# Optimization experiments

Measured on AMD Instinct MI355X. Metric: run time of the kernel, lower is better.

Reference implementation:

```python
import jax, jax.numpy as jnp
import numpy as np

B, S, H, HKV, D = 2, 1024, 32, 8, 128


def _rope_tables(seq_len, head_dim, base=10000.0):
    inv_freq = 1.0 / (base ** (np.arange(0, head_dim, 2, dtype=np.float32) / head_dim))
    freqs = np.arange(seq_len, dtype=np.float32)[:, None] * inv_freq[None, :]  # [S, D/2]
    emb = np.concatenate([freqs, freqs], axis=-1)  # [S, D] (Llama layout)
    return jnp.asarray(np.cos(emb)), jnp.asarray(np.sin(emb))


def setup_inputs() -> dict:
    key = jax.random.key(0)
    kq, kk, kv = jax.random.split(key, 3)
    q = jax.random.normal(kq, (B, S, H, D), dtype=jnp.float32)
    k = jax.random.normal(kk, (B, S, HKV, D), dtype=jnp.float32)
    v = jax.random.normal(kv, (B, S, HKV, D), dtype=jnp.float32)
    cos, sin = _rope_tables(S, D)
    # additive causal mask [B, 1, S, S]: 0 where allowed, large negative where masked
    causal = jnp.tril(jnp.ones((S, S), dtype=bool))
    mask = jnp.where(causal, 0.0, -1e9).astype(jnp.float32)
    attention_mask = jnp.broadcast_to(mask[None, None], (B, 1, S, S))
    softmax_scale = 1.0 / float(np.sqrt(D))
    return {
        "query_states": q, "key_states": k, "value_states": v,
        "cos": cos, "sin": sin, "attention_mask": attention_mask,
        "softmax_scale": softmax_scale,
    }


def _apply_rope(x, cos, sin):
    # x: [B, S, h, D]; cos/sin: [S, D]
    d2 = x.shape[-1] // 2
    rot = jnp.concatenate([-x[..., d2:], x[..., :d2]], axis=-1)  # rotate_half
    return x * cos[None, :, None, :] + rot * sin[None, :, None, :]


def reference(query_states, key_states, value_states, cos, sin, attention_mask, softmax_scale):
    b, s, h, d = query_states.shape
    hkv = key_states.shape[2]
    g = h // hkv  # GQA group size
    q = _apply_rope(query_states, cos, sin)
    k = _apply_rope(key_states, cos, sin)
    qg = q.reshape(b, s, hkv, g, d)
    # scores: [B, Hkv, G, Q, K]
    scores = jnp.einsum('bqhgd,bkhd->bhgqk', qg, k) * softmax_scale
    scores = scores + attention_mask[:, :, None]  # [B,1,Q,K] -> broadcast over (Hkv, G)
    p = jax.nn.softmax(scores, axis=-1)
    out = jnp.einsum('bhgqk,bkhd->bqhgd', p, value_states)
    return out.reshape(b, s, h, d)
```

## Files before the change

kernel.cpp:

```cpp
#include <hip/hip_runtime.h>

#define S_LEN 1024
#define D_DIM 128
#define NH    32
#define NKV   8
#define NB    2

typedef __bf16 bf16x8 __attribute__((ext_vector_type(8)));
typedef float  f32x16 __attribute__((ext_vector_type(16)));
typedef unsigned short u16x8 __attribute__((ext_vector_type(8)));
typedef unsigned int   u32x4 __attribute__((ext_vector_type(4)));

__device__ __forceinline__ unsigned short f2bf(float f) {
    unsigned int u = __float_as_uint(f);
    u += 0x7fffu + ((u >> 16) & 1u);
    return (unsigned short)(u >> 16);
}

__device__ __forceinline__ void gld_lds16(const unsigned short* g, unsigned short* l) {
    __builtin_amdgcn_global_load_lds(
        (const __attribute__((address_space(1))) unsigned int*)(g),
        (__attribute__((address_space(3))) unsigned int*)(l), 16, 0, 0);
}

__global__ __launch_bounds__(256) void rope_q_kernel(
    const float* __restrict__ q, const float* __restrict__ cosb,
    const float* __restrict__ sinb, const float* __restrict__ scale_ptr,
    unsigned short* __restrict__ Qr)
{
    const float sc = *scale_ptr * 1.44269504088896f;
    int gid = blockIdx.x * 256 + threadIdx.x;
    int row = gid >> 6;
    int j   = gid & 63;
    int h  = row & (NH - 1);
    int bs = row >> 5;
    int s  = bs & (S_LEN - 1);
    int b  = bs >> 10;
    const float* qp = q + (size_t)row * D_DIM;
    float x0 = qp[j];
    float x1 = qp[j + 64];
    float c  = cosb[s * D_DIM + j];
    float sn = sinb[s * D_DIM + j];
    size_t orow = ((size_t)(b * NH + h) * S_LEN + s) * D_DIM;
    Qr[orow + j]      = f2bf((x0 * c - x1 * sn) * sc);
    Qr[orow + j + 64] = f2bf((x1 * c + x0 * sn) * sc);
}

__global__ __launch_bounds__(256) void rope_k_kernel(
    const float* __restrict__ k, const float* __restrict__ cosb,
    const float* __restrict__ sinb, unsigned short* __restrict__ Kr)
{
    int gid = blockIdx.x * 256 + threadIdx.x;
    int row = gid >> 6;
    int j   = gid & 63;
    int hk = row & (NKV - 1);
    int bs = row >> 3;
    int s  = bs & (S_LEN - 1);
    int b  = bs >> 10;
    const float* kp = k + (size_t)row * D_DIM;
    float x0 = kp[j];
    float x1 = kp[j + 64];
    float c  = cosb[s * D_DIM + j];
    float sn = sinb[s * D_DIM + j];
    size_t orow = ((size_t)(b * NKV + hk) * S_LEN + s) * D_DIM;
    Kr[orow + j]      = f2bf(x0 * c - x1 * sn);
    Kr[orow + j + 64] = f2bf(x1 * c + x0 * sn);
}

__global__ __launch_bounds__(256) void transpose_v_kernel(
    const float* __restrict__ v, unsigned short* __restrict__ Vt)
{
    int blk   = blockIdx.x;
    int stile = blk & 15;
    int hk    = (blk >> 4) & (NKV - 1);
    int b     = blk >> 7;
    int tid   = threadIdx.x;
    __shared__ __align__(16) unsigned short tile[64][132];
#pragma unroll
    for (int i = 0; i < 8; i++) {
        int e    = i * 256 + tid;
        int srow = e >> 5;
        int dq   = (e & 31) * 4;
        const float* vp = v + (((size_t)(b * S_LEN + stile * 64 + srow) * NKV + hk) * D_DIM + dq);
        float4 val = *(const float4*)vp;
        tile[srow][dq + 0] = f2bf(val.x);
        tile[srow][dq + 1] = f2bf(val.y);
        tile[srow][dq + 2] = f2bf(val.z);
        tile[srow][dq + 3] = f2bf(val.w);
    }
    __syncthreads();
    size_t head = (size_t)(b * NKV + hk) * D_DIM * S_LEN;
#pragma unroll
    for (int i = 0; i < 4; i++) {
        int g  = i * 256 + tid;
        int d  = g >> 3;
        int c8 = g & 7;
        int s0 = c8 * 8;
        u16x8 pk;
#pragma unroll
        for (int jj = 0; jj < 8; jj++) pk[jj] = tile[s0 + jj][d];
        *(u16x8*)(Vt + head + (size_t)d * S_LEN + stile * 64 + s0) = pk;
    }
}

__global__ __launch_bounds__(512, 2) void attn_kernel(
    const unsigned short* __restrict__ Qr,
    const unsigned short* __restrict__ Kr,
    const unsigned short* __restrict__ Vt,
    float* __restrict__ out)
{
    const int bid = blockIdx.x;
    const int swz = (bid & 7) * 32 + (bid >> 3);
    const int t  = swz & 3;
    const int h  = (swz >> 2) & 31;
    const int b  = swz >> 7;
    const int hk = h >> 2;

    const int tid  = threadIdx.x;
    const int w    = tid >> 6;
    const int lane = tid & 63;
    const int ln   = lane & 31;
    const int hi   = lane >> 5;

    __shared__ __align__(16) unsigned short Kt[2][64 * 128];
    __shared__ __align__(16) unsigned short Vs[2][128 * 64];

    const int q0 = t * 256 + w * 32;
    const int qg = q0 + ln;

    const unsigned short* khead = Kr + (size_t)(b * NKV + hk) * S_LEN * D_DIM;
    const unsigned short* vhead = Vt + (size_t)(b * NKV + hk) * D_DIM * S_LEN;

    const int krow = lane >> 4;
    const int kcc  = lane & 15;
    const int vrw  = lane >> 3;
    const int vcc  = lane & 7;

    auto stage = [&](int u, int buf) {
        const unsigned short* kt = khead + (size_t)u * 64 * D_DIM;
#pragma unroll
        for (int n = 0; n < 2; n++) {
            int row = w * 8 + n * 4 + krow;
            int cc  = kcc ^ (row & 7);
            gld_lds16(kt + (size_t)row * D_DIM + cc * 8, &Kt[buf][(w * 8 + n * 4) * 128]);
        }
        const unsigned short* vt = vhead + (size_t)u * 64;
#pragma unroll
        for (int n = 0; n < 2; n++) {
            int d  = w * 16 + n * 8 + vrw;
            int cc = vcc ^ (d & 7);
            gld_lds16(vt + (size_t)d * S_LEN + cc * 8, &Vs[buf][(w * 16 + n * 8) * 64]);
        }
    };

    const unsigned short* qrow =
        Qr + ((size_t)(b * NH + h) * S_LEN + qg) * D_DIM + hi * 8;
    bf16x8 qf[8];
#pragma unroll
    for (int dd = 0; dd < 8; dd++)
        qf[dd] = *(const bf16x8*)(qrow + dd * 16);

    f32x16 o[4];
#pragma unroll
    for (int dt = 0; dt < 4; dt++)
#pragma unroll
        for (int r = 0; r < 16; r++) o[dt][r] = 0.f;
    float m_run = -1e30f, lsum = 0.f;

    const int U = 4 * t + 4;
    stage(0, 0);

#pragma unroll 1
    for (int u = 0; u < U; ++u) {
        const int cur = u & 1;
        __syncthreads();
        if (u + 1 < U) stage(u + 1, cur ^ 1);

        if (64 * u <= q0 + 31) {
            const bool act1 = (64 * u + 32 <= q0 + 31);

            f32x16 st[2];
#pragma unroll
            for (int r = 0; r < 16; r++) { st[0][r] = 0.f; st[1][r] = 0.f; }
            __builtin_amdgcn_s_setprio(1);
#pragma unroll
            for (int s = 0; s < 2; s++) {
                if (s == 0 || act1) {
#pragma unroll
                    for (int dd = 0; dd < 8; dd++) {
                        int row = s * 32 + ln;
                        int c   = (2 * dd + hi) ^ (row & 7);
                        bf16x8 kf = *(const bf16x8*)(&Kt[cur][row * 128 + c * 8]);
                        st[s] = __builtin_amdgcn_mfma_f32_32x32x16_bf16(kf, qf[dd], st[s], 0, 0, 0);
                    }
                }
            }
            __builtin_amdgcn_s_setprio(0);

            if (64 * u + 63 > q0) {
#pragma unroll
                for (int s = 0; s < 2; s++)
#pragma unroll
                    for (int r = 0; r < 16; r++) {
                        int kg = 64 * u + 32 * s + (r & 3) + 8 * (r >> 2) + 4 * hi;
                        if (kg > qg) st[s][r] = -1e30f;
                    }
            }

            float mx = -1e30f;
#pragma unroll
            for (int r = 0; r < 16; r++) mx = fmaxf(mx, st[0][r]);
            if (act1) {
#pragma unroll
                for (int r = 0; r < 16; r++) mx = fmaxf(mx, st[1][r]);
            }
            float pm = fmaxf(mx, __shfl_xor(mx, 32));

            if (__any(pm > m_run + 8.f)) {
                float mnew = fmaxf(m_run, pm);
                float ps   = exp2f(m_run - mnew);
                m_run = mnew;
                lsum *= ps;
#pragma unroll
                for (int r = 0; r < 16; r++) {
                    float psr = __shfl(ps, (r & 3) + 8 * (r >> 2) + 4 * hi);
#pragma unroll
                    for (int dt = 0; dt < 4; dt++) o[dt][r] *= psr;
                }
            }
            float ls = 0.f;
#pragma unroll
            for (int r = 0; r < 16; r++) {
                float p = exp2f(st[0][r] - m_run);
                st[0][r] = p; ls += p;
            }
            if (act1) {
#pragma unroll
                for (int r = 0; r < 16; r++) {
                    float p = exp2f(st[1][r] - m_run);
                    st[1][r] = p; ls += p;
                }
            }
            lsum += ls + __shfl_xor(ls, 32);

            const char* vbase = (const char*)&Vs[cur][0];
            __builtin_amdgcn_s_setprio(1);
#pragma unroll
            for (int ks = 0; ks < 4; ks++) {
                if (ks < 2 || act1) {
                    const f32x16& sv = st[ks >> 1];
                    const int g = (ks & 1) * 8;
                    unsigned int d0 = (unsigned)f2bf(sv[g + 0]) | ((unsigned)f2bf(sv[g + 1]) << 16);
                    unsigned int d1 = (unsigned)f2bf(sv[g + 2]) | ((unsigned)f2bf(sv[g + 3]) << 16);
                    unsigned int d2 = (unsigned)f2bf(sv[g + 4]) | ((unsigned)f2bf(sv[g + 5]) << 16);
                    unsigned int d3 = (unsigned)f2bf(sv[g + 6]) | ((unsigned)f2bf(sv[g + 7]) << 16);
                    u32x4 paw = {d0, d1, d2, d3};
                    bf16x8 pa = __builtin_bit_cast(bf16x8, paw);
#pragma unroll
                    for (int dt = 0; dt < 4; dt++) {
                        int d = dt * 32 + ln;
                        const char* vrow = vbase + d * 128;
                        int x = d & 7;
                        uint2 vlo = *(const uint2*)(vrow + (((2 * ks)     ^ x) * 16) + hi * 8);
                        uint2 vhi = *(const uint2*)(vrow + (((2 * ks + 1) ^ x) * 16) + hi * 8);
                        u32x4 vw = {vlo.x, vlo.y, vhi.x, vhi.y};
                        bf16x8 vf = __builtin_bit_cast(bf16x8, vw);
                        o[dt] = __builtin_amdgcn_mfma_f32_32x32x16_bf16(pa, vf, o[dt], 0, 0, 0);
                    }
                }
            }
            __builtin_amdgcn_s_setprio(0);
        }
    }

    float rcp = 1.0f / lsum;
    float* ob = out + ((size_t)(b * S_LEN + q0) * NH + h) * D_DIM;
#pragma unroll
    for (int r = 0; r < 16; r++) {
        int qo = (r & 3) + 8 * (r >> 2) + 4 * hi;
        float invr = __shfl(rcp, qo);
#pragma unroll
        for (int dt = 0; dt < 4; dt++)
            ob[(size_t)qo * NH * D_DIM + dt * 32 + ln] = o[dt][r] * invr;
    }
}

extern "C" void kernel_launch(void* const* d_in, const int* in_sizes, int n_in,
                              void* d_out, int out_size, void* d_ws, size_t ws_size,
                              hipStream_t stream) {
    const float* q    = (const float*)d_in[0];
    const float* k    = (const float*)d_in[1];
    const float* v    = (const float*)d_in[2];
    const float* cosb = (const float*)d_in[3];
    const float* sinb = (const float*)d_in[4];
    const float* scale = (const float*)d_in[6];
    float* out = (float*)d_out;

    unsigned short* Qr = (unsigned short*)d_ws;
    unsigned short* Kr = Qr + (size_t)NB * NH  * S_LEN * D_DIM;
    unsigned short* Vt = Kr + (size_t)NB * NKV * S_LEN * D_DIM;

    rope_q_kernel<<<NB * S_LEN * NH / 4, 256, 0, stream>>>(q, cosb, sinb, scale, Qr);
    rope_k_kernel<<<NB * S_LEN * NKV / 4, 256, 0, stream>>>(k, cosb, sinb, Kr);
    transpose_v_kernel<<<NB * NKV * (S_LEN / 64), 256, 0, stream>>>(v, Vt);
    attn_kernel<<<NB * NH * (S_LEN / 256), 512, 0, stream>>>(Qr, Kr, Vt, out);
}
```

Before: 77.05 us.

## Fuse Q RoPE into attention, merge K/V prep, triple-buffer with paired causal tiles

Removes the separate Q RoPE kernel: each attention wave now loads fp32 Q, cos and sin directly, applies RoPE and the softmax scale, and converts to bf16 in registers. K RoPE and the V transpose are merged into one launch, so the pipeline drops from four launches to two. The attention kernel switches to 256-thread blocks that each handle two 128-row query tiles (qt = 7-pr and qt = pr) to balance causal work, and uses a three-stage K/V LDS ring with explicit vmcnt waits. Costs are a larger LDS footprint, only 256 blocks in the grid, and Q RoPE inputs read in fp32 inside the main kernel.

```diff
diff --git a/kernel.cpp b/kernel.cpp
--- a/kernel.cpp
+++ b/kernel.cpp
@@ -23,98 +23,76 @@
         (__attribute__((address_space(3))) unsigned int*)(l), 16, 0, 0);
 }
 
-__global__ __launch_bounds__(256) void rope_q_kernel(
-    const float* __restrict__ q, const float* __restrict__ cosb,
-    const float* __restrict__ sinb, const float* __restrict__ scale_ptr,
-    unsigned short* __restrict__ Qr)
+__global__ __launch_bounds__(256) void prep_kv_kernel(
+    const float* __restrict__ k, const float* __restrict__ cosb,
+    const float* __restrict__ sinb, const float* __restrict__ v,
+    unsigned short* __restrict__ Kr, unsigned short* __restrict__ Vt)
 {
-    const float sc = *scale_ptr * 1.44269504088896f;
-    int gid = blockIdx.x * 256 + threadIdx.x;
-    int row = gid >> 6;
-    int j   = gid & 63;
-    int h  = row & (NH - 1);
-    int bs = row >> 5;
-    int s  = bs & (S_LEN - 1);
-    int b  = bs >> 10;
-    const float* qp = q + (size_t)row * D_DIM;
-    float x0 = qp[j];
-    float x1 = qp[j + 64];
-    float c  = cosb[s * D_DIM + j];
-    float sn = sinb[s * D_DIM + j];
-    size_t orow = ((size_t)(b * NH + h) * S_LEN + s) * D_DIM;
-    Qr[orow + j]      = f2bf((x0 * c - x1 * sn) * sc);
-    Qr[orow + j + 64] = f2bf((x1 * c + x0 * sn) * sc);
-}
-
-__global__ __launch_bounds__(256) void rope_k_kernel(
-    const float* __restrict__ k, const float* __restrict__ cosb,
-    const float* __restrict__ sinb, unsigned short* __restrict__ Kr)
-{
-    int gid = blockIdx.x * 256 + threadIdx.x;
-    int row = gid >> 6;
-    int j   = gid & 63;
-    int hk = row & (NKV - 1);
-    int bs = row >> 3;
-    int s  = bs & (S_LEN - 1);
-    int b  = bs >> 10;
-    const float* kp = k + (size_t)row * D_DIM;
-    float x0 = kp[j];
-    float x1 = kp[j + 64];
-    float c  = cosb[s * D_DIM + j];
-    float sn = sinb[s * D_DIM + j];
-    size_t orow = ((size_t)(b * NKV + hk) * S_LEN + s) * D_DIM;
-    Kr[orow + j]      = f2bf(x0 * c - x1 * sn);
-    Kr[orow + j + 64] = f2bf(x1 * c + x0 * sn);
-}
-
-__global__ __launch_bounds__(256) void transpose_v_kernel(
-    const float* __restrict__ v, unsigned short* __restrict__ Vt)
-{
-    int blk   = blockIdx.x;
-    int stile = blk & 15;
-    int hk    = (blk >> 4) & (NKV - 1);
-    int b     = blk >> 7;
-    int tid   = threadIdx.x;
+    const int tid = threadIdx.x;
     __shared__ __align__(16) unsigned short tile[64][132];
-#pragma unroll
-    for (int i = 0; i < 8; i++) {
-        int e    = i * 256 + tid;
-        int srow = e >> 5;
-        int dq   = (e & 31) * 4;
-        const float* vp = v + (((size_t)(b * S_LEN + stile * 64 + srow) * NKV + hk) * D_DIM + dq);
-        float4 val = *(const float4*)vp;
-        tile[srow][dq + 0] = f2bf(val.x);
-        tile[srow][dq + 1] = f2bf(val.y);
-        tile[srow][dq + 2] = f2bf(val.z);
-        tile[srow][dq + 3] = f2bf(val.w);
+    if (blockIdx.x < 4096) {
+        int gid = blockIdx.x * 256 + tid;
+        int row = gid >> 6;
+        int j   = gid & 63;
+        int hk = row & (NKV - 1);
+        int bs = row >> 3;
+        int s  = bs & (S_LEN - 1);
+        int b  = bs >> 10;
+        const float* kp = k + (size_t)row * D_DIM;
+        float x0 = kp[j];
+        float x1 = kp[j + 64];
+        float c  = cosb[s * D_DIM + j];
+        float sn = sinb[s * D_DIM + j];
+        size_t orow = ((size_t)(b * NKV + hk) * S_LEN + s) * D_DIM;
+        Kr[orow + j]      = f2bf(x0 * c - x1 * sn);
+        Kr[orow + j + 64] = f2bf(x1 * c + x0 * sn);
+    } else {
+        int blk   = blockIdx.x - 4096;
+        int stile = blk & 15;
+        int hk    = (blk >> 4) & (NKV - 1);
+        int b     = blk >> 7;
+#pragma unroll
+        for (int i = 0; i < 8; i++) {
+            int e    = i * 256 + tid;
+            int srow = e >> 5;
+            int dq   = (e & 31) * 4;
+            const float* vp = v + (((size_t)(b * S_LEN + stile * 64 + srow) * NKV + hk) * D_DIM + dq);
+            float4 val = *(const float4*)vp;
+            tile[srow][dq + 0] = f2bf(val.x);
+            tile[srow][dq + 1] = f2bf(val.y);
+            tile[srow][dq + 2] = f2bf(val.z);
+            tile[srow][dq + 3] = f2bf(val.w);
+        }
+        __syncthreads();
+        size_t head = (size_t)(b * NKV + hk) * D_DIM * S_LEN;
+#pragma unroll
+        for (int i = 0; i < 4; i++) {
+            int g  = i * 256 + tid;
+            int d  = g >> 3;
+            int c8 = g & 7;
+            int s0 = c8 * 8;
+            u16x8 pk;
+#pragma unroll
+            for (int jj = 0; jj < 8; jj++) pk[jj] = tile[s0 + jj][d];
+            *(u16x8*)(Vt + head + (size_t)d * S_LEN + stile * 64 + s0) = pk;
+        }
     }
-    __syncthreads();
-    size_t head = (size_t)(b * NKV + hk) * D_DIM * S_LEN;
-#pragma unroll
-    for (int i = 0; i < 4; i++) {
-        int g  = i * 256 + tid;
-        int d  = g >> 3;
-        int c8 = g & 7;
-        int s0 = c8 * 8;
-        u16x8 pk;
-#pragma unroll
-        for (int jj = 0; jj < 8; jj++) pk[jj] = tile[s0 + jj][d];
-        *(u16x8*)(Vt + head + (size_t)d * S_LEN + stile * 64 + s0) = pk;
-    }
-}
-
-__global__ __launch_bounds__(512, 2) void attn_kernel(
-    const unsigned short* __restrict__ Qr,
+}
+
+__global__ __launch_bounds__(256) void attn_kernel(
+    const float* __restrict__ qraw,
     const unsigned short* __restrict__ Kr,
     const unsigned short* __restrict__ Vt,
+    const float* __restrict__ cosb, const float* __restrict__ sinb,
+    const float* __restrict__ scale_ptr,
     float* __restrict__ out)
 {
-    const int bid = blockIdx.x;
-    const int swz = (bid & 7) * 32 + (bid >> 3);
-    const int t  = swz & 3;
-    const int h  = (swz >> 2) & 31;
-    const int b  = swz >> 7;
-    const int hk = h >> 2;
+    const int bid  = blockIdx.x;
+    const int pr   = bid & 3;
+    const int head = bid >> 2;
+    const int h    = head & 31;
+    const int b    = head >> 5;
+    const int hk   = h >> 2;
 
     const int tid  = threadIdx.x;
     const int w    = tid >> 6;
@@ -122,11 +100,10 @@
     const int ln   = lane & 31;
     const int hi   = lane >> 5;
 
-    __shared__ __align__(16) unsigned short Kt[2][64 * 128];
-    __shared__ __align__(16) unsigned short Vs[2][128 * 64];
-
-    const int q0 = t * 256 + w * 32;
-    const int qg = q0 + ln;
+    const float sc = *scale_ptr * 1.44269504088896f;
+
+    __shared__ __align__(16) unsigned short Kt[3][64 * 128];
+    __shared__ __align__(16) unsigned short Vs[3][128 * 64];
 
     const unsigned short* khead = Kr + (size_t)(b * NKV + hk) * S_LEN * D_DIM;
     const unsigned short* vhead = Vt + (size_t)(b * NKV + hk) * D_DIM * S_LEN;
@@ -139,149 +116,182 @@
     auto stage = [&](int u, int buf) {
         const unsigned short* kt = khead + (size_t)u * 64 * D_DIM;
 #pragma unroll
-        for (int n = 0; n < 2; n++) {
-            int row = w * 8 + n * 4 + krow;
+        for (int n = 0; n < 4; n++) {
+            int row = w * 16 + n * 4 + krow;
             int cc  = kcc ^ (row & 7);
-            gld_lds16(kt + (size_t)row * D_DIM + cc * 8, &Kt[buf][(w * 8 + n * 4) * 128]);
+            gld_lds16(kt + (size_t)row * D_DIM + cc * 8, &Kt[buf][(w * 16 + n * 4) * 128]);
         }
         const unsigned short* vt = vhead + (size_t)u * 64;
 #pragma unroll
-        for (int n = 0; n < 2; n++) {
-            int d  = w * 16 + n * 8 + vrw;
+        for (int n = 0; n < 4; n++) {
+            int d  = w * 32 + n * 8 + vrw;
             int cc = vcc ^ (d & 7);
-            gld_lds16(vt + (size_t)d * S_LEN + cc * 8, &Vs[buf][(w * 16 + n * 8) * 64]);
+            gld_lds16(vt + (size_t)d * S_LEN + cc * 8, &Vs[buf][(w * 32 + n * 8) * 64]);
         }
     };
 
-    const unsigned short* qrow =
-        Qr + ((size_t)(b * NH + h) * S_LEN + qg) * D_DIM + hi * 8;
-    bf16x8 qf[8];
-#pragma unroll
-    for (int dd = 0; dd < 8; dd++)
-        qf[dd] = *(const bf16x8*)(qrow + dd * 16);
-
-    f32x16 o[4];
-#pragma unroll
-    for (int dt = 0; dt < 4; dt++)
-#pragma unroll
-        for (int r = 0; r < 16; r++) o[dt][r] = 0.f;
-    float m_run = -1e30f, lsum = 0.f;
-
-    const int U = 4 * t + 4;
-    stage(0, 0);
-
 #pragma unroll 1
-    for (int u = 0; u < U; ++u) {
-        const int cur = u & 1;
-        __syncthreads();
-        if (u + 1 < U) stage(u + 1, cur ^ 1);
-
-        if (64 * u <= q0 + 31) {
-            const bool act1 = (64 * u + 32 <= q0 + 31);
-
-            f32x16 st[2];
-#pragma unroll
-            for (int r = 0; r < 16; r++) { st[0][r] = 0.f; st[1][r] = 0.f; }
-            __builtin_amdgcn_s_setprio(1);
-#pragma unroll
-            for (int s = 0; s < 2; s++) {
-                if (s == 0 || act1) {
-#pragma unroll
-                    for (int dd = 0; dd < 8; dd++) {
-                        int row = s * 32 + ln;
-                        int c   = (2 * dd + hi) ^ (row & 7);
-                        bf16x8 kf = *(const bf16x8*)(&Kt[cur][row * 128 + c * 8]);
-                        st[s] = __builtin_amdgcn_mfma_f32_32x32x16_bf16(kf, qf[dd], st[s], 0, 0, 0);
+    for (int pass = 0; pass < 2; ++pass) {
+        const int qt = pass ? pr : (7 - pr);
+        const int U  = 2 * qt + 2;
+        const int q0 = qt * 128 + w * 32;
+        const int qg = q0 + ln;
+
+        const float* qrowf = qraw + (((size_t)(b * S_LEN + qg)) * NH + h) * D_DIM;
+        const float* ct = cosb + (size_t)qg * D_DIM;
+        const float* st_ = sinb + (size_t)qg * D_DIM;
+        bf16x8 qf[8];
+#pragma unroll
+        for (int dd = 0; dd < 4; dd++) {
+            int b0 = dd * 16 + hi * 8;
+            int b1 = b0 + 64;
+            float4 x0a = *(const float4*)(qrowf + b0), x0b = *(const float4*)(qrowf + b0 + 4);
+            float4 x1a = *(const float4*)(qrowf + b1), x1b = *(const float4*)(qrowf + b1 + 4);
+            float4 c0a = *(const float4*)(ct + b0),  c0b = *(const float4*)(ct + b0 + 4);
+            float4 c1a = *(const float4*)(ct + b1),  c1b = *(const float4*)(ct + b1 + 4);
+            float4 s0a = *(const float4*)(st_ + b0), s0b = *(const float4*)(st_ + b0 + 4);
+            float4 s1a = *(const float4*)(st_ + b1), s1b = *(const float4*)(st_ + b1 + 4);
+            u16x8 lo, hi8;
+#pragma unroll
+            for (int j = 0; j < 4; j++) {
+                float xl0 = ((const float*)&x0a)[j], xh0 = ((const float*)&x1a)[j];
+                lo[j]  = f2bf((xl0 * ((const float*)&c0a)[j] - xh0 * ((const float*)&s0a)[j]) * sc);
+                hi8[j] = f2bf((xh0 * ((const float*)&c1a)[j] + xl0 * ((const float*)&s1a)[j]) * sc);
+                float xl1 = ((const float*)&x0b)[j], xh1 = ((const float*)&x1b)[j];
+                lo[j + 4]  = f2bf((xl1 * ((const float*)&c0b)[j] - xh1 * ((const float*)&s0b)[j]) * sc);
+                hi8[j + 4] = f2bf((xh1 * ((const float*)&c1b)[j] + xl1 * ((const float*)&s1b)[j]) * sc);
+            }
+            qf[dd]     = __builtin_bit_cast(bf16x8, lo);
+            qf[dd + 4] = __builtin_bit_cast(bf16x8, hi8);
+        }
+
+        f32x16 o[4];
+#pragma unroll
+        for (int dt = 0; dt < 4; dt++)
+#pragma unroll
+            for (int r = 0; r < 16; r++) o[dt][r] = 0.f;
+        float m_run = -1e30f, lsum = 0.f;
+
+        if (pass) __builtin_amdgcn_s_barrier();
+        stage(0, 0);
+        stage(1, 1);
+
+#pragma unroll 1
+        for (int u = 0; u < U; ++u) {
+            const int cur = u % 3;
+            if (u + 1 < U) asm volatile("s_waitcnt vmcnt(8)" ::: "memory");
+            else           asm volatile("s_waitcnt vmcnt(0)" ::: "memory");
+            __builtin_amdgcn_s_barrier();
+            __builtin_amdgcn_sched_barrier(0);
+            if (u + 2 < U) stage(u + 2, (u + 2) % 3);
+
+            if (64 * u <= q0 + 31) {
+                const bool act1 = (64 * u + 32 <= q0 + 31);
+
+                f32x16 st[2];
+#pragma unroll
+                for (int r = 0; r < 16; r++) { st[0][r] = 0.f; st[1][r] = 0.f; }
+                __builtin_amdgcn_s_setprio(1);
+#pragma unroll
+                for (int s = 0; s < 2; s++) {
+                    if (s == 0 || act1) {
+#pragma unroll
+                        for (int dd = 0; dd < 8; dd++) {
+                            int row = s * 32 + ln;
+                            int c   = (2 * dd + hi) ^ (row & 7);
+                            bf16x8 kf = *(const bf16x8*)(&Kt[cur][row * 128 + c * 8]);
+                            st[s] = __builtin_amdgcn_mfma_f32_32x32x16_bf16(kf, qf[dd], st[s], 0, 0, 0);
+                        }
                     }
                 }
+                __builtin_amdgcn_s_setprio(0);
+
+                if (64 * u + 63 > q0) {
+#pragma unroll
+                    for (int s = 0; s < 2; s++)
+#pragma unroll
+                        for (int r = 0; r < 16; r++) {
+                            int kg = 64 * u + 32 * s + (r & 3) + 8 * (r >> 2) + 4 * hi;
+                            if (kg > qg) st[s][r] = -1e30f;
+                        }
+                }
+
+                float mx = -1e30f;
+#pragma unroll
+                for (int r = 0; r < 16; r++) mx = fmaxf(mx, st[0][r]);
+                if (act1) {
+#pragma unroll
+                    for (int r = 0; r < 16; r++) mx = fmaxf(mx, st[1][r]);
+                }
+                float pm = fmaxf(mx, __shfl_xor(mx, 32));
+
+                if (__any(pm > m_run + 8.f)) {
+                    float mnew = fmaxf(m_run, pm);
+                    float ps   = exp2f(m_run - mnew);
+                    m_run = mnew;
+                    lsum *= ps;
+#pragma unroll
+                    for (int r = 0; r < 16; r++) {
+                        float psr = __shfl(ps, (r & 3) + 8 * (r >> 2) + 4 * hi);
+#pragma unroll
+                        for (int dt = 0; dt < 4; dt++) o[dt][r] *= psr;
+                    }
+                }
+                float ls = 0.f;
+#pragma unroll
+                for (int r = 0; r < 16; r++) {
+                    float p = exp2f(st[0][r] - m_run);
+                    st[0][r] = p; ls += p;
+                }
+                if (act1) {
+#pragma unroll
+                    for (int r = 0; r < 16; r++) {
+                        float p = exp2f(st[1][r] - m_run);
+                        st[1][r] = p; ls += p;
+                    }
+                }
+                lsum += ls + __shfl_xor(ls, 32);
+
+                const char* vbase = (const char*)&Vs[cur][0];
+                __builtin_amdgcn_s_setprio(1);
+#pragma unroll
+                for (int ks = 0; ks < 4; ks++) {
+                    if (ks < 2 || act1) {
+                        const f32x16& sv = st[ks >> 1];
+                        const int g = (ks & 1) * 8;
+                        unsigned int d0 = (unsigned)f2bf(sv[g + 0]) | ((unsigned)f2bf(sv[g + 1]) << 16);
+                        unsigned int d1 = (unsigned)f2bf(sv[g + 2]) | ((unsigned)f2bf(sv[g + 3]) << 16);
+                        unsigned int d2 = (unsigned)f2bf(sv[g + 4]) | ((unsigned)f2bf(sv[g + 5]) << 16);
+                        unsigned int d3 = (unsigned)f2bf(sv[g + 6]) | ((unsigned)f2bf(sv[g + 7]) << 16);
+                        u32x4 paw = {d0, d1, d2, d3};
+                        bf16x8 pa = __builtin_bit_cast(bf16x8, paw);
+#pragma unroll
+                        for (int dt = 0; dt < 4; dt++) {
+                            int d = dt * 32 + ln;
+                            const char* vrow = vbase + d * 128;
+                            int x = d & 7;
+                            uint2 vlo = *(const uint2*)(vrow + (((2 * ks)     ^ x) * 16) + hi * 8);
+                            uint2 vhi = *(const uint2*)(vrow + (((2 * ks + 1) ^ x) * 16) + hi * 8);
+                            u32x4 vw = {vlo.x, vlo.y, vhi.x, vhi.y};
+                            bf16x8 vf = __builtin_bit_cast(bf16x8, vw);
+                            o[dt] = __builtin_amdgcn_mfma_f32_32x32x16_bf16(pa, vf, o[dt], 0, 0, 0);
+                        }
+                    }
+                }
+                __builtin_amdgcn_s_setprio(0);
             }
-            __builtin_amdgcn_s_setprio(0);
-
-            if (64 * u + 63 > q0) {
-#pragma unroll
-                for (int s = 0; s < 2; s++)
-#pragma unroll
-                    for (int r = 0; r < 16; r++) {
-                        int kg = 64 * u + 32 * s + (r & 3) + 8 * (r >> 2) + 4 * hi;
-                        if (kg > qg) st[s][r] = -1e30f;
-                    }
-            }
-
-            float mx = -1e30f;
-#pragma unroll
-            for (int r = 0; r < 16; r++) mx = fmaxf(mx, st[0][r]);
-            if (act1) {
-#pragma unroll
-                for (int r = 0; r < 16; r++) mx = fmaxf(mx, st[1][r]);
-            }
-            float pm = fmaxf(mx, __shfl_xor(mx, 32));
-
-            if (__any(pm > m_run + 8.f)) {
-                float mnew = fmaxf(m_run, pm);
-                float ps   = exp2f(m_run - mnew);
-                m_run = mnew;
-                lsum *= ps;
-#pragma unroll
-                for (int r = 0; r < 16; r++) {
-                    float psr = __shfl(ps, (r & 3) + 8 * (r >> 2) + 4 * hi);
-#pragma unroll
-                    for (int dt = 0; dt < 4; dt++) o[dt][r] *= psr;
-                }
-            }
-            float ls = 0.f;
-#pragma unroll
-            for (int r = 0; r < 16; r++) {
-                float p = exp2f(st[0][r] - m_run);
-                st[0][r] = p; ls += p;
-            }
-            if (act1) {
-#pragma unroll
-                for (int r = 0; r < 16; r++) {
-                    float p = exp2f(st[1][r] - m_run);
-                    st[1][r] = p; ls += p;
-                }
-            }
-            lsum += ls + __shfl_xor(ls, 32);
-
-            const char* vbase = (const char*)&Vs[cur][0];
-            __builtin_amdgcn_s_setprio(1);
-#pragma unroll
-            for (int ks = 0; ks < 4; ks++) {
-                if (ks < 2 || act1) {
-                    const f32x16& sv = st[ks >> 1];
-                    const int g = (ks & 1) * 8;
-                    unsigned int d0 = (unsigned)f2bf(sv[g + 0]) | ((unsigned)f2bf(sv[g + 1]) << 16);
-                    unsigned int d1 = (unsigned)f2bf(sv[g + 2]) | ((unsigned)f2bf(sv[g + 3]) << 16);
-                    unsigned int d2 = (unsigned)f2bf(sv[g + 4]) | ((unsigned)f2bf(sv[g + 5]) << 16);
-                    unsigned int d3 = (unsigned)f2bf(sv[g + 6]) | ((unsigned)f2bf(sv[g + 7]) << 16);
-                    u32x4 paw = {d0, d1, d2, d3};
-                    bf16x8 pa = __builtin_bit_cast(bf16x8, paw);
-#pragma unroll
-                    for (int dt = 0; dt < 4; dt++) {
-                        int d = dt * 32 + ln;
-                        const char* vrow = vbase + d * 128;
-                        int x = d & 7;
-                        uint2 vlo = *(const uint2*)(vrow + (((2 * ks)     ^ x) * 16) + hi * 8);
-                        uint2 vhi = *(const uint2*)(vrow + (((2 * ks + 1) ^ x) * 16) + hi * 8);
-                        u32x4 vw = {vlo.x, vlo.y, vhi.x, vhi.y};
-                        bf16x8 vf = __builtin_bit_cast(bf16x8, vw);
-                        o[dt] = __builtin_amdgcn_mfma_f32_32x32x16_bf16(pa, vf, o[dt], 0, 0, 0);
-                    }
-                }
-            }
-            __builtin_amdgcn_s_setprio(0);
-        }
-    }
-
-    float rcp = 1.0f / lsum;
-    float* ob = out + ((size_t)(b * S_LEN + q0) * NH + h) * D_DIM;
-#pragma unroll
-    for (int r = 0; r < 16; r++) {
-        int qo = (r & 3) + 8 * (r >> 2) + 4 * hi;
-        float invr = __shfl(rcp, qo);
-#pragma unroll
-        for (int dt = 0; dt < 4; dt++)
-            ob[(size_t)qo * NH * D_DIM + dt * 32 + ln] = o[dt][r] * invr;
+        }
+
+        float rcp = 1.0f / lsum;
+        float* ob = out + ((size_t)(b * S_LEN + q0) * NH + h) * D_DIM;
+#pragma unroll
+        for (int r = 0; r < 16; r++) {
+            int qo = (r & 3) + 8 * (r >> 2) + 4 * hi;
+            float invr = __shfl(rcp, qo);
+#pragma unroll
+            for (int dt = 0; dt < 4; dt++)
+                ob[(size_t)qo * NH * D_DIM + dt * 32 + ln] = o[dt][r] * invr;
+        }
     }
 }
 
@@ -296,12 +306,9 @@
     const float* scale = (const float*)d_in[6];
     float* out = (float*)d_out;
 
-    unsigned short* Qr = (unsigned short*)d_ws;
-    unsigned short* Kr = Qr + (size_t)NB * NH  * S_LEN * D_DIM;
+    unsigned short* Kr = (unsigned short*)d_ws;
     unsigned short* Vt = Kr + (size_t)NB * NKV * S_LEN * D_DIM;
 
-    rope_q_kernel<<<NB * S_LEN * NH / 4, 256, 0, stream>>>(q, cosb, sinb, scale, Qr);
-    rope_k_kernel<<<NB * S_LEN * NKV / 4, 256, 0, stream>>>(k, cosb, sinb, Kr);
-    transpose_v_kernel<<<NB * NKV * (S_LEN / 64), 256, 0, stream>>>(v, Vt);
-    attn_kernel<<<NB * NH * (S_LEN / 256), 512, 0, stream>>>(Qr, Kr, Vt, out);
-}
+    prep_kv_kernel<<<4096 + 256, 256, 0, stream>>>(k, cosb, sinb, v, Kr, Vt);
+    attn_kernel<<<256, 256, 0, stream>>>(q, Kr, Vt, cosb, sinb, scale, out);
+}
```

Measured after the change: 81.35 us. +5.6%, slower.
